# Kernel tuning notes

Measured on AMD Instinct MI355X. Metric: run time of the kernel, lower is better.

## Reference

```python
import jax, jax.numpy as jnp
import numpy as np

N, M, D = 131072, 32, 32


def setup_inputs() -> dict:
    key = jax.random.key(0)
    k1, k2, k3, k4 = jax.random.split(key, 4)
    # scale points/centers so Mahalanobis distances are O(1) and exp(-d) is well-conditioned
    points = 0.2 * jax.random.normal(k1, (N, D), dtype=jnp.float32)
    centers = 0.2 * jax.random.normal(k2, (M, D), dtype=jnp.float32)
    covs_inv_sqrt = jnp.eye(D, dtype=jnp.float32)[None] + 0.05 * jax.random.normal(k3, (M, D, D), dtype=jnp.float32)
    weights = jax.random.normal(k4, (M,), dtype=jnp.float32)
    return {"points": points, "centers": centers, "covs_inv_sqrt": covs_inv_sqrt, "weights": weights}


def reference(points, centers, covs_inv_sqrt, weights):
    # refresh(): covs_inv = L @ L^T, coefs = softmax(weights) * sqrt(det(covs_inv))
    A = jnp.einsum('mdk,mek->mde', covs_inv_sqrt, covs_inv_sqrt)  # (M, D, D)
    coefs = jax.nn.softmax(weights) * jnp.sqrt(jnp.linalg.det(A))  # (M,)

    # weightedsqdist: d_nm = (x_n - c_m)^T A_m (x_n - c_m), expanded to avoid (N,M,D) diff
    xAx = jnp.einsum('nd,mde,ne->nm', points, A, points)          # (N, M)
    Ac = jnp.einsum('mde,me->md', A, centers)                     # (M, D)
    xAc = jnp.einsum('nd,md->nm', points, Ac)                     # (N, M)
    cAc = jnp.einsum('md,md->m', centers, Ac)                     # (M,)
    dists = xAx - 2.0 * xAc + cAc[None, :]

    # coefs * exp(-dists) with mixture reduction over centers (KeOps sum over j)
    return jnp.exp(-dists) @ coefs  # (N,)
```

## Files before the change

### kernel.cpp

```cpp
#include <hip/hip_runtime.h>
#include <hip/hip_bf16.h>


#define D 32
#define M 32
#define WT 2

typedef __attribute__((ext_vector_type(8))) short short8;
typedef __attribute__((ext_vector_type(4))) float f32x4;

__device__ __forceinline__ unsigned short f2bf_rne(float f) {
  unsigned int u = __float_as_uint(f);
  return (unsigned short)((u + 0x7FFFu + ((u >> 16) & 1u)) >> 16);
}

#define DPP_ADD(x, ctrl) \
  ((x) + __int_as_float(__builtin_amdgcn_mov_dpp(__float_as_int(x), (ctrl), 0xf, 0xf, true)))

#define SCL 1.2011224087864498f

__global__ __launch_bounds__(64) void gmm_pre(
    const float* __restrict__ centers, const float* __restrict__ L,
    const float* __restrict__ weights,
    float2* __restrict__ CN, float* __restrict__ LC,
    unsigned short* __restrict__ LH, unsigned short* __restrict__ LL) {
  __shared__ float U[D][D + 1];
  __shared__ float C2s[D];
  const int m = blockIdx.x;
  const int t = threadIdx.x;
  const float* Lm = L + m * (D * D);

  if (t < D) {
    for (int k = 0; k < D; ++k) U[t][k] = Lm[t * D + k];
    float acc = 0.f;
    for (int d = 0; d < D; ++d) acc = fmaf(centers[m * D + d], Lm[d * D + t], acc);
    C2s[t] = acc;
  }

  {
    const int col = t & 15;
    const int dbase = 8 * (t >> 4);
    for (int kt = 0; kt < 2; ++kt) {
      for (int j = 0; j < 8; ++j) {
        const int d = dbase + j;
        const int k = kt * 16 + col;
        float v = Lm[d * D + k] * SCL;
        unsigned int hi = __float_as_uint(v) & 0xFFFF0000u;
        float lo = v - __uint_as_float(hi);
        size_t off = (((size_t)(m * 2 + kt)) * 64 + t) * 8 + j;
        LH[off] = (unsigned short)(hi >> 16);
        LL[off] = f2bf_rne(lo);
      }
    }
  }
  __syncthreads();

  CN[m * 64 + t] = make_float2(-SCL * C2s[t & 15], -SCL * C2s[16 + (t & 15)]);

  for (int p = 0; p < D - 1; ++p) {
    if (t > p && t < D) {
      float f = U[t][p] / U[p][p];
      for (int k = p; k < D; ++k) U[t][k] -= f * U[p][k];
    }
    __syncthreads();
  }
  if (t == 0) {
    float det = 1.f;
    for (int i = 0; i < D; ++i) det *= U[i][i];
    float mx = -1e30f;
    for (int j = 0; j < M; ++j) mx = fmaxf(mx, weights[j]);
    float s = 0.f;
    for (int j = 0; j < M; ++j) s += __expf(weights[j] - mx);
    float coef = (__expf(weights[m] - mx) / s) * fabsf(det);
    LC[m] = log2f(coef);
  }
}

__global__ __launch_bounds__(256) void gmm_main(
    const float* __restrict__ points,
    const float2* __restrict__ CN, const float* __restrict__ LC,
    const unsigned short* __restrict__ LH, const unsigned short* __restrict__ LL,
    float* __restrict__ out, int N) {
  const int lane = threadIdx.x & 63;
  const int wave = threadIdx.x >> 6;
  const int col = lane & 15;
  const int g = lane >> 4;
  const int tileBase = (blockIdx.x * 4 + wave) * (WT * 16);
  if (tileBase >= N) return;

  const bool b0 = (lane >> 2) & 1;
  const bool b1 = (lane >> 2) & 2;

  short8 xh[WT], xl[WT];
#pragma unroll
  for (int t = 0; t < WT; ++t) {
    const float* p = points + (size_t)(tileBase + t * 16 + col) * D + 8 * g;
    float4 a = *reinterpret_cast<const float4*>(p);
    float4 b = *reinterpret_cast<const float4*>(p + 4);
    float v[8] = {a.x, a.y, a.z, a.w, b.x, b.y, b.z, b.w};
    unsigned int hiu[8];
    unsigned int lou[8];
#pragma unroll
    for (int j = 0; j < 8; ++j) {
      unsigned int u = __float_as_uint(v[j]);
      hiu[j] = u & 0xFFFF0000u;
      lou[j] = __float_as_uint(v[j] - __uint_as_float(hiu[j]));
    }
    union { short8 s; unsigned int w[4]; } H, Lo;
#pragma unroll
    for (int jj = 0; jj < 4; ++jj) {
      H.w[jj]  = __builtin_amdgcn_perm(hiu[2 * jj + 1], hiu[2 * jj], 0x07060302);
      Lo.w[jj] = __builtin_amdgcn_perm(lou[2 * jj + 1], lou[2 * jj], 0x07060302);
    }
    xh[t] = H.s;
    xl[t] = Lo.s;
  }

  float result[WT];
#pragma unroll
  for (int t = 0; t < WT; ++t) result[t] = 0.f;

  const short8* bh_base = reinterpret_cast<const short8*>(LH);
  const short8* bl_base = reinterpret_cast<const short8*>(LL);

#pragma unroll 4
  for (int m = 0; m < M; ++m) {
    short8 bh0 = bh_base[(m * 2 + 0) * 64 + lane];
    short8 bh1 = bh_base[(m * 2 + 1) * 64 + lane];
    short8 bl0 = bl_base[(m * 2 + 0) * 64 + lane];
    short8 bl1 = bl_base[(m * 2 + 1) * 64 + lane];
    const float2 cn = CN[m * 64 + lane];
    const float lc = LC[m];

#pragma unroll
    for (int t = 0; t < WT; ++t) {
      f32x4 acc0 = (f32x4){cn.x, cn.x, cn.x, cn.x};
      f32x4 acc1 = (f32x4){cn.y, cn.y, cn.y, cn.y};
      acc0 = __builtin_amdgcn_mfma_f32_16x16x32_bf16(xh[t], bh0, acc0, 0, 0, 0);
      acc0 = __builtin_amdgcn_mfma_f32_16x16x32_bf16(xl[t], bh0, acc0, 0, 0, 0);
      acc0 = __builtin_amdgcn_mfma_f32_16x16x32_bf16(xh[t], bl0, acc0, 0, 0, 0);
      acc1 = __builtin_amdgcn_mfma_f32_16x16x32_bf16(xh[t], bh1, acc1, 0, 0, 0);
      acc1 = __builtin_amdgcn_mfma_f32_16x16x32_bf16(xl[t], bh1, acc1, 0, 0, 0);
      acc1 = __builtin_amdgcn_mfma_f32_16x16x32_bf16(xh[t], bl1, acc1, 0, 0, 0);

      float sq0, sq1, sq2, sq3;
      {
        float s0 = fmaf(acc0[0], acc0[0], acc1[0] * acc1[0]);
        float s1 = fmaf(acc0[1], acc0[1], acc1[1] * acc1[1]);
        float s2 = fmaf(acc0[2], acc0[2], acc1[2] * acc1[2]);
        float s3 = fmaf(acc0[3], acc0[3], acc1[3] * acc1[3]);
        s0 = DPP_ADD(s0, 0x128); s0 = DPP_ADD(s0, 0x124);
        s1 = DPP_ADD(s1, 0x128); s1 = DPP_ADD(s1, 0x124);
        s2 = DPP_ADD(s2, 0x128); s2 = DPP_ADD(s2, 0x124);
        s3 = DPP_ADD(s3, 0x128); s3 = DPP_ADD(s3, 0x124);
        sq0 = s0; sq1 = s1; sq2 = s2; sq3 = s3;
      }
      float v = b1 ? (b0 ? sq3 : sq2) : (b0 ? sq1 : sq0);
      v = DPP_ADD(v, 0xB1);
      v = DPP_ADD(v, 0x4E);
      result[t] += exp2f(lc - v);
    }
  }

  if ((lane & 3) == 0) {
    const int q = (lane >> 2) & 3;
#pragma unroll
    for (int t = 0; t < WT; ++t)
      out[tileBase + t * 16 + 4 * g + q] = result[t];
  }
}

extern "C" void kernel_launch(void* const* d_in, const int* in_sizes, int n_in,
                              void* d_out, int out_size, void* d_ws, size_t ws_size,
                              hipStream_t stream) {
  const float* points  = (const float*)d_in[0];
  const float* centers = (const float*)d_in[1];
  const float* L       = (const float*)d_in[2];
  const float* weights = (const float*)d_in[3];
  float* out = (float*)d_out;
  const int N = in_sizes[0] / D;

  char* ws = (char*)d_ws;
  float2* CN          = (float2*)ws;
  float* LC           = (float*)(ws + 16384);
  unsigned short* LHf = (unsigned short*)(ws + 32768);
  unsigned short* LLf = (unsigned short*)(ws + 98304);

  gmm_pre<<<M, 64, 0, stream>>>(centers, L, weights, CN, LC, LHf, LLf);

  const int ptsPerBlock = 4 * WT * 16;
  gmm_main<<<(N + ptsPerBlock - 1) / ptsPerBlock, 256, 0, stream>>>(
      points, CN, LC, LHf, LLf, out, N);
}
```

Measured before the change: 122.1 us.

## Stage precomputed bf16 factor tiles in LDS shared by 1024-thread blocks

The main kernel now uses 1024-thread blocks of 16 waves. Each block first copies the whole hi/lo bf16 split of L (128KB) and a compacted center-projection table into LDS, then every wave reads its MFMA B operands from LDS instead of global memory. The center-projection buffer shrinks from 64 to 16 float2 per center, and each lane indexes it by column. The goal is to stop every wave from streaming the full 128KB factor set through the cache hierarchy. In exchange, LDS use near the per-CU limit allows only one block per CU, the copy is not overlapped with compute, and the N bound check is removed, so N must be a multiple of 512.

```diff
diff --git a/kernel.cpp b/kernel.cpp
--- a/kernel.cpp
+++ b/kernel.cpp
@@ -22,7 +22,7 @@
 __global__ __launch_bounds__(64) void gmm_pre(
     const float* __restrict__ centers, const float* __restrict__ L,
     const float* __restrict__ weights,
-    float2* __restrict__ CN, float* __restrict__ LC,
+    float2* __restrict__ CNp, float* __restrict__ LC,
     unsigned short* __restrict__ LH, unsigned short* __restrict__ LL) {
   __shared__ float U[D][D + 1];
   __shared__ float C2s[D];
@@ -55,7 +55,7 @@
   }
   __syncthreads();
 
-  CN[m * 64 + t] = make_float2(-SCL * C2s[t & 15], -SCL * C2s[16 + (t & 15)]);
+  if (t < 16) CNp[m * 16 + t] = make_float2(-SCL * C2s[t], -SCL * C2s[16 + t]);
 
   for (int p = 0; p < D - 1; ++p) {
     if (t > p && t < D) {
@@ -76,17 +76,34 @@
   }
 }
 
-__global__ __launch_bounds__(256) void gmm_main(
+__global__ __launch_bounds__(1024, 4) void gmm_main(
     const float* __restrict__ points,
-    const float2* __restrict__ CN, const float* __restrict__ LC,
+    const float2* __restrict__ CNp, const float* __restrict__ LC,
     const unsigned short* __restrict__ LH, const unsigned short* __restrict__ LL,
     float* __restrict__ out, int N) {
-  const int lane = threadIdx.x & 63;
-  const int wave = threadIdx.x >> 6;
+  __shared__ unsigned short sLH[M * 2 * 64 * 8];
+  __shared__ unsigned short sLL[M * 2 * 64 * 8];
+  __shared__ float2 sCN[M * 16];
+
+  const int tid = threadIdx.x;
+  const int lane = tid & 63;
+  const int wave = tid >> 6;
   const int col = lane & 15;
   const int g = lane >> 4;
-  const int tileBase = (blockIdx.x * 4 + wave) * (WT * 16);
-  if (tileBase >= N) return;
+
+  {
+    const uint4* src = reinterpret_cast<const uint4*>(LH);
+    uint4* dst = reinterpret_cast<uint4*>(sLH);
+#pragma unroll
+    for (int i = 0; i < 4; ++i) dst[tid + i * 1024] = src[tid + i * 1024];
+    src = reinterpret_cast<const uint4*>(LL);
+    dst = reinterpret_cast<uint4*>(sLL);
+#pragma unroll
+    for (int i = 0; i < 4; ++i) dst[tid + i * 1024] = src[tid + i * 1024];
+    if (tid < M * 16) sCN[tid] = CNp[tid];
+  }
+
+  const int tileBase = (blockIdx.x * 16 + wave) * (WT * 16);
 
   const bool b0 = (lane >> 2) & 1;
   const bool b1 = (lane >> 2) & 2;
@@ -116,20 +133,22 @@
     xl[t] = Lo.s;
   }
 
+  __syncthreads();
+
   float result[WT];
 #pragma unroll
   for (int t = 0; t < WT; ++t) result[t] = 0.f;
 
-  const short8* bh_base = reinterpret_cast<const short8*>(LH);
-  const short8* bl_base = reinterpret_cast<const short8*>(LL);
-
-#pragma unroll 4
+  const short8* bh_base = reinterpret_cast<const short8*>(sLH);
+  const short8* bl_base = reinterpret_cast<const short8*>(sLL);
+
+#pragma unroll 2
   for (int m = 0; m < M; ++m) {
     short8 bh0 = bh_base[(m * 2 + 0) * 64 + lane];
     short8 bh1 = bh_base[(m * 2 + 1) * 64 + lane];
     short8 bl0 = bl_base[(m * 2 + 0) * 64 + lane];
     short8 bl1 = bl_base[(m * 2 + 1) * 64 + lane];
-    const float2 cn = CN[m * 64 + lane];
+    const float2 cn = sCN[m * 16 + col];
     const float lc = LC[m];
 
 #pragma unroll
@@ -143,19 +162,15 @@
       acc1 = __builtin_amdgcn_mfma_f32_16x16x32_bf16(xl[t], bh1, acc1, 0, 0, 0);
       acc1 = __builtin_amdgcn_mfma_f32_16x16x32_bf16(xh[t], bl1, acc1, 0, 0, 0);
 
-      float sq0, sq1, sq2, sq3;
-      {
-        float s0 = fmaf(acc0[0], acc0[0], acc1[0] * acc1[0]);
-        float s1 = fmaf(acc0[1], acc0[1], acc1[1] * acc1[1]);
-        float s2 = fmaf(acc0[2], acc0[2], acc1[2] * acc1[2]);
-        float s3 = fmaf(acc0[3], acc0[3], acc1[3] * acc1[3]);
-        s0 = DPP_ADD(s0, 0x128); s0 = DPP_ADD(s0, 0x124);
-        s1 = DPP_ADD(s1, 0x128); s1 = DPP_ADD(s1, 0x124);
-        s2 = DPP_ADD(s2, 0x128); s2 = DPP_ADD(s2, 0x124);
-        s3 = DPP_ADD(s3, 0x128); s3 = DPP_ADD(s3, 0x124);
-        sq0 = s0; sq1 = s1; sq2 = s2; sq3 = s3;
-      }
-      float v = b1 ? (b0 ? sq3 : sq2) : (b0 ? sq1 : sq0);
+      float s0 = fmaf(acc0[0], acc0[0], acc1[0] * acc1[0]);
+      float s1 = fmaf(acc0[1], acc0[1], acc1[1] * acc1[1]);
+      float s2 = fmaf(acc0[2], acc0[2], acc1[2] * acc1[2]);
+      float s3 = fmaf(acc0[3], acc0[3], acc1[3] * acc1[3]);
+      s0 = DPP_ADD(s0, 0x128); s0 = DPP_ADD(s0, 0x124);
+      s1 = DPP_ADD(s1, 0x128); s1 = DPP_ADD(s1, 0x124);
+      s2 = DPP_ADD(s2, 0x128); s2 = DPP_ADD(s2, 0x124);
+      s3 = DPP_ADD(s3, 0x128); s3 = DPP_ADD(s3, 0x124);
+      float v = b1 ? (b0 ? s3 : s2) : (b0 ? s1 : s0);
       v = DPP_ADD(v, 0xB1);
       v = DPP_ADD(v, 0x4E);
       result[t] += exp2f(lc - v);
@@ -181,14 +196,13 @@
   const int N = in_sizes[0] / D;
 
   char* ws = (char*)d_ws;
-  float2* CN          = (float2*)ws;
-  float* LC           = (float*)(ws + 16384);
-  unsigned short* LHf = (unsigned short*)(ws + 32768);
-  unsigned short* LLf = (unsigned short*)(ws + 98304);
-
-  gmm_pre<<<M, 64, 0, stream>>>(centers, L, weights, CN, LC, LHf, LLf);
-
-  const int ptsPerBlock = 4 * WT * 16;
-  gmm_main<<<(N + ptsPerBlock - 1) / ptsPerBlock, 256, 0, stream>>>(
-      points, CN, LC, LHf, LLf, out, N);
-}
+  float2* CNp         = (float2*)ws;
+  float* LC           = (float*)(ws + 4096);
+  unsigned short* LHf = (unsigned short*)(ws + 8192);
+  unsigned short* LLf = (unsigned short*)(ws + 8192 + 65536);
+
+  gmm_pre<<<M, 64, 0, stream>>>(centers, L, weights, CNp, LC, LHf, LLf);
+
+  gmm_main<<<N / (16 * WT * 16), 1024, 0, stream>>>(
+      points, CNp, LC, LHf, LLf, out, N);
+}
```

Result: no change. 119.8 us (-1.8%).
